# Kernel optimization log

Hardware: AMD Instinct MI355X
Metric: run time of the kernel (lower is better)

## Reference

```python
import jax, jax.numpy as jnp
import numpy as np
import math

B, S, E, H = 2, 2048, 768, 12
D = E // H            # head_dim = 64
FFN = 3072            # GeGLU hidden
WIN = 64              # local window size
GLOBAL_IDS = np.array([0])
EPS = 1e-5


def _rope(x):
    # x: [B,H,S,D]; interleaved rotary embedding, theta=10000 (lucidrains RotaryEmbedding)
    d = x.shape[-1]
    s = x.shape[-2]
    inv_freq = 1.0 / (10000.0 ** (jnp.arange(0, d, 2, dtype=jnp.float32) / d))
    freqs = jnp.arange(s, dtype=jnp.float32)[:, None] * inv_freq[None, :]  # [S, D/2]
    freqs = jnp.repeat(freqs, 2, axis=-1)                                   # [S, D]
    cos, sin = jnp.cos(freqs), jnp.sin(freqs)
    xp = x.reshape(x.shape[:-1] + (d // 2, 2))
    x_rot = jnp.stack([-xp[..., 1], xp[..., 0]], axis=-1).reshape(x.shape)
    return x * cos + x_rot * sin


def _layernorm(x, scale, bias):
    mu = jnp.mean(x, axis=-1, keepdims=True)
    var = jnp.mean(jnp.square(x - mu), axis=-1, keepdims=True)
    return (x - mu) * jax.lax.rsqrt(var + EPS) * scale + bias


def setup_inputs() -> dict:
    key = jax.random.key(0)
    ks = jax.random.split(key, 10)
    def xav(k, shape, gain):
        fan_out, fan_in = shape
        std = gain * math.sqrt(2.0 / (fan_in + fan_out))
        return jax.random.normal(k, shape, jnp.float32) * std
    g2 = math.sqrt(2.0)
    g13 = math.sqrt(1.0 / 3.0)
    return {
        "x": jax.random.normal(ks[0], (B, S, E), jnp.float32),
        "rel_pos_bias": jax.random.normal(ks[1], (B, S, S), jnp.float32),
        "mask": jnp.ones((B, S), dtype=bool),
        "wq_w": xav(ks[2], (E, E), g2), "wq_b": jnp.zeros((E,), jnp.float32),
        "wk_w": xav(ks[3], (E, E), g2), "wk_b": jnp.zeros((E,), jnp.float32),
        "wv_w": xav(ks[4], (E, E), g2), "wv_b": jnp.zeros((E,), jnp.float32),
        "fc_w": xav(ks[5], (E, E), g2), "fc_b": jnp.zeros((E,), jnp.float32),
        "pos_coeff": jnp.full((H, 1, 1), 0.01, jnp.float32),
        "gate_w": xav(ks[6], (FFN, E), g13), "gate_b": jnp.zeros((FFN,), jnp.float32),
        "value_w": xav(ks[7], (FFN, E), g2), "value_b": jnp.zeros((FFN,), jnp.float32),
        "down_w": xav(ks[8], (E, FFN), g2), "down_b": jnp.zeros((E,), jnp.float32),
        "ln1_s": jnp.ones((E,), jnp.float32), "ln1_b": jnp.zeros((E,), jnp.float32),
        "ln2_s": jnp.ones((E,), jnp.float32), "ln2_b": jnp.zeros((E,), jnp.float32),
    }


def _sparse_allow(mask):
    # static local-window + global-token pattern, [S,S] bool
    idx = jnp.arange(S)
    allow = jnp.abs(idx[:, None] - idx[None, :]) <= WIN
    gidx = jnp.asarray(GLOBAL_IDS)
    allow = allow.at[gidx, :].set(True)
    allow = allow.at[:, gidx].set(True)
    # combine with padding mask [B,S] broadcast over query rows
    return allow[None, None, :, :] & mask[:, None, None, :]  # [B,1,S,S]


def reference(x, rel_pos_bias, mask, wq_w, wq_b, wk_w, wk_b, wv_w, wv_b,
              fc_w, fc_b, pos_coeff, gate_w, gate_b, value_w, value_b,
              down_w, down_b, ln1_s, ln1_b, ln2_s, ln2_b):
    def heads(t):  # [B,S,E] -> [B,H,S,D]
        return t.reshape(B, S, H, D).transpose(0, 2, 1, 3)

    Q = _rope(heads(x @ wq_w.T + wq_b))
    K = _rope(heads(x @ wk_w.T + wk_b))
    V = heads(x @ wv_w.T + wv_b)

    scores = jnp.einsum('bhqd,bhkd->bhqk', Q, K) / math.sqrt(D)
    scores = scores + pos_coeff[None] * rel_pos_bias[:, None]     # [B,H,S,S]
    allow = _sparse_allow(mask)
    scores = jnp.where(allow, scores, -1e30)
    scores = scores - jnp.max(scores, axis=-1, keepdims=True)
    attn = jax.nn.softmax(scores, axis=-1)
    ctx = jnp.einsum('bhqk,bhkd->bhqd', attn, V)
    ctx = ctx.transpose(0, 2, 1, 3).reshape(B, S, E)
    attn_out = ctx @ fc_w.T + fc_b

    h = _layernorm(x + attn_out, ln1_s, ln1_b)
    gate = jax.nn.gelu(h @ gate_w.T + gate_b, approximate=False)
    ffn = (gate * (h @ value_w.T + value_b)) @ down_w.T + down_b
    return _layernorm(h + ffn, ln2_s, ln2_b)
```

## Files before the change

### kernel.cpp

```cpp
#include <hip/hip_runtime.h>
#include <math.h>

#define B_   2
#define S_   2048
#define E_   768
#define H_   12
#define D_   64
#define FFN_ 3072
#define WIN_ 64
#define MTOT (B_*S_)

typedef unsigned short ushort_t;
typedef unsigned short ushort8 __attribute__((ext_vector_type(8)));
typedef __bf16 bf16x8 __attribute__((ext_vector_type(8)));
typedef float f32x4 __attribute__((ext_vector_type(4)));
typedef _Float16 half_t;

__device__ __forceinline__ float b2f(ushort_t u) {
    union { unsigned int i; float f; } c; c.i = ((unsigned int)u) << 16; return c.f;
}
__device__ __forceinline__ ushort_t f2b(float f) {
    union { float f; unsigned int i; } c; c.f = f;
    unsigned int u = c.i;
    return (ushort_t)((u + 0x7fffu + ((u >> 16) & 1u)) >> 16);
}
__device__ __forceinline__ float gelu_f(float g) {
    return 0.5f * g * (1.f + erff(g * 0.70710678118654752440f));
}

typedef const __attribute__((address_space(1))) void* gptr_t;
typedef __attribute__((address_space(3))) void* lptr_t;
__device__ __forceinline__ void gload16(const void* g, void* l) {
    __builtin_amdgcn_global_load_lds((gptr_t)g,
        (lptr_t)(unsigned int)(unsigned long long)l, 16, 0, 0);
}

__global__ __launch_bounds__(256)
void cvt_f32_bf16(const float* __restrict__ in, ushort_t* __restrict__ out, int n8)
{
    const int idx = blockIdx.x * 256 + threadIdx.x;
    if (idx >= n8) return;
    const float4* p = (const float4*)(in + (size_t)idx * 8);
    const float4 a = p[0], b = p[1];
    ushort8 o;
    o[0]=f2b(a.x); o[1]=f2b(a.y); o[2]=f2b(a.z); o[3]=f2b(a.w);
    o[4]=f2b(b.x); o[5]=f2b(b.y); o[6]=f2b(b.z); o[7]=f2b(b.w);
    *(ushort8*)(out + (size_t)idx*8) = o;
}

__global__ __launch_bounds__(256)
void cvt_interleave(const float* __restrict__ gw, const float* __restrict__ vw,
                    ushort_t* __restrict__ out)
{
    const int idx = blockIdx.x*256 + threadIdx.x;
    const int R   = idx / 96, c8 = idx - R*96;
    const int blk = R >> 6, w = R & 63;
    const float* src = (w < 32 ? gw : vw) + (size_t)(blk*32 + (w & 31))*768 + c8*8;
    const float4 a = ((const float4*)src)[0], b = ((const float4*)src)[1];
    ushort8 o;
    o[0]=f2b(a.x); o[1]=f2b(a.y); o[2]=f2b(a.z); o[3]=f2b(a.w);
    o[4]=f2b(b.x); o[5]=f2b(b.y); o[6]=f2b(b.z); o[7]=f2b(b.w);
    *(ushort8*)(out + (size_t)idx*8) = o;
}

__global__ __launch_bounds__(256)
void rope_table(float2* __restrict__ ctab)
{
    const int idx = blockIdx.x*256 + threadIdx.x;
    if (idx >= S_*32) return;
    const int s = idx >> 5, i = idx & 31;
    const float inv = exp2f(-(float)i * (13.287712379549449f/32.0f));
    const float fr = (float)s * inv;
    ctab[idx] = make_float2(cosf(fr), sinf(fr));
}

template<int EPI, int BN>
__global__ __launch_bounds__(256)
void gemm_mfma(const ushort_t* __restrict__ A,
               const ushort_t* W0, const float* b0, void* C0,
               const ushort_t* W1, const float* b1, void* C1,
               const ushort_t* W2, const float* b2, void* C2,
               const void* __restrict__ aux, int M, int N, int K)
{
    constexpr int NWC = BN/64, NWR = 4/NWC, WROWS = 128/NWR, MF = WROWS/16;
    const ushort_t* W = W0; const float* bias = b0; void* C = C0;
    if (blockIdx.z == 1) { W = W1; bias = b1; C = C1; }
    else if (blockIdx.z == 2) { W = W2; bias = b2; C = C2; }

    __shared__ __align__(16) ushort_t As[128*32];
    __shared__ __align__(16) ushort_t Bs[BN*32];

    const int tid = threadIdx.x, wv = tid>>6, lane = tid&63;
    const int m0 = blockIdx.y*128, n0 = blockIdx.x*BN;
    const int wr = wv / NWC, wc = wv % NWC;
    const int lr16 = lane & 15, lkb = (lane>>4)<<3;

    f32x4 acc[MF][4];
#pragma unroll
    for (int i=0;i<MF;++i)
#pragma unroll
        for (int j=0;j<4;++j) acc[i][j] = f32x4{0.f,0.f,0.f,0.f};

    const char* Ab = (const char*)(A + (size_t)m0*K);
    const char* Wb = (const char*)(W + (size_t)n0*K);
    const size_t rb = (size_t)K*2;
    const int wbase = wv*1024, lby = lane*16;

    for (int kt = 0; kt < K; kt += 32) {
        const size_t kb = (size_t)kt*2;
        int n_ = wbase + lby;
        gload16(Ab + (size_t)(n_>>6)*rb + kb + (n_&63), (char*)As + wbase);
        n_ += 4096;
        gload16(Ab + (size_t)(n_>>6)*rb + kb + (n_&63), (char*)As + wbase + 4096);
        n_ = wbase + lby;
        gload16(Wb + (size_t)(n_>>6)*rb + kb + (n_&63), (char*)Bs + wbase);
        if (BN == 128) {
            n_ += 4096;
            gload16(Wb + (size_t)(n_>>6)*rb + kb + (n_&63), (char*)Bs + wbase + 4096);
        }
        __syncthreads();
        bf16x8 af[MF], bfr[4];
#pragma unroll
        for (int mf=0; mf<MF; ++mf)
            af[mf] = *(const bf16x8*)&As[(wr*WROWS + mf*16 + lr16)*32 + lkb];
#pragma unroll
        for (int nf=0; nf<4; ++nf)
            bfr[nf] = *(const bf16x8*)&Bs[(wc*64 + nf*16 + lr16)*32 + lkb];
#pragma unroll
        for (int mf=0; mf<MF; ++mf)
#pragma unroll
            for (int nf=0; nf<4; ++nf)
                acc[mf][nf] = __builtin_amdgcn_mfma_f32_16x16x32_bf16(af[mf], bfr[nf], acc[mf][nf], 0,0,0);
        __syncthreads();
    }

    const int colb = n0 + wc*64 + lr16;
    const int rowb = m0 + wr*WROWS + ((lane>>4)<<2);
#pragma unroll
    for (int nf=0; nf<4; ++nf) {
        const int col = colb + nf*16;
        const float bsv = bias[col];
#pragma unroll
        for (int mf=0; mf<MF; ++mf) {
            const int row = rowb + mf*16;
            const f32x4 a = acc[mf][nf];
#pragma unroll
            for (int r=0; r<4; ++r) {
                const size_t off = (size_t)(row+r)*N + col;
                const float v = a[r] + bsv;
                if constexpr (EPI == 0) {
                    ((ushort_t*)C)[off] = f2b(v);
                } else {
                    ((float*)C)[off] = v + ((const float*)aux)[off];
                }
            }
        }
// ... 43 lines not shown

#define STGQ(tt, cb) { \
    char* dA = lds + (cb)*BUFB + wv*2048; \
    char* dB = lds + (cb)*BUFB + ABY + wv*2048; \
    const size_t ko = (size_t)(tt)*64; \
    gload16(Agp + ko,           dA); \
    gload16(Agp + ko + 16*1536, dA + 1024); \
    gload16(Bgp + ko,           dB); \
    gload16(Bgp + ko + 16*1536, dB + 1024); }

    STGQ(0, 0);
    __syncthreads();

    int c = 0;
#pragma unroll 1
    for (int t = 0; t < NT; ++t) {
        if (t < NT-1) STGQ(t+1, c^1);
        const char* Lb = lds + c*BUFB;
        const bf16x8 a0 = *(const bf16x8*)(Lb + rA0 + ck);
        const bf16x8 a1 = *(const bf16x8*)(Lb + rA1 + ck);
        const bf16x8 a2 = *(const bf16x8*)(Lb + rA2 + ck);
        const bf16x8 a3 = *(const bf16x8*)(Lb + rA3 + ck);
        const bf16x8 b0 = *(const bf16x8*)(Lb + rB0 + ck);
        const bf16x8 b1 = *(const bf16x8*)(Lb + rB1 + ck);
        const bf16x8 b2 = *(const bf16x8*)(Lb + rB2 + ck);
        const bf16x8 b3 = *(const bf16x8*)(Lb + rB3 + ck);
        __builtin_amdgcn_s_setprio(1);
        acc[0][0] = __builtin_amdgcn_mfma_f32_16x16x32_bf16(a0, b0, acc[0][0], 0,0,0);
        acc[1][0] = __builtin_amdgcn_mfma_f32_16x16x32_bf16(a1, b0, acc[1][0], 0,0,0);
        acc[2][0] = __builtin_amdgcn_mfma_f32_16x16x32_bf16(a2, b0, acc[2][0], 0,0,0);
        acc[3][0] = __builtin_amdgcn_mfma_f32_16x16x32_bf16(a3, b0, acc[3][0], 0,0,0);
        acc[0][1] = __builtin_amdgcn_mfma_f32_16x16x32_bf16(a0, b1, acc[0][1], 0,0,0);
        acc[1][1] = __builtin_amdgcn_mfma_f32_16x16x32_bf16(a1, b1, acc[1][1], 0,0,0);
        acc[2][1] = __builtin_amdgcn_mfma_f32_16x16x32_bf16(a2, b1, acc[2][1], 0,0,0);
        acc[3][1] = __builtin_amdgcn_mfma_f32_16x16x32_bf16(a3, b1, acc[3][1], 0,0,0);
        acc[0][2] = __builtin_amdgcn_mfma_f32_16x16x32_bf16(a0, b2, acc[0][2], 0,0,0);
        acc[1][2] = __builtin_amdgcn_mfma_f32_16x16x32_bf16(a1, b2, acc[1][2], 0,0,0);
        acc[2][2] = __builtin_amdgcn_mfma_f32_16x16x32_bf16(a2, b2, acc[2][2], 0,0,0);
        acc[3][2] = __builtin_amdgcn_mfma_f32_16x16x32_bf16(a3, b2, acc[3][2], 0,0,0);
        acc[0][3] = __builtin_amdgcn_mfma_f32_16x16x32_bf16(a0, b3, acc[0][3], 0,0,0);
        acc[1][3] = __builtin_amdgcn_mfma_f32_16x16x32_bf16(a1, b3, acc[1][3], 0,0,0);
        acc[2][3] = __builtin_amdgcn_mfma_f32_16x16x32_bf16(a2, b3, acc[2][3], 0,0,0);
        acc[3][3] = __builtin_amdgcn_mfma_f32_16x16x32_bf16(a3, b3, acc[3][3], 0,0,0);
        __builtin_amdgcn_s_setprio(0);
        __syncthreads();
        c ^= 1;
    }
#undef STGQ

    const int tsel = gx / 6;
    const float* bias = (tsel==0) ? bq : (tsel==1) ? bk : bv;
    ushort_t* out = (tsel==0) ? Qb : Kb;
    const int colb = (gx - tsel*6)*128 + wc*64 + lr16;
    const int rowb = m0 + wr*64 + ((l>>4)<<2);
#pragma unroll
    for (int nf=0; nf<4; ++nf) {
        const int col = colb + nf*16;
        const float bsv = bias[col];
#pragma unroll
        for (int mf=0; mf<4; ++mf) {
            const int row = rowb + mf*16;
            const f32x4 a = acc[mf][nf];
#pragma unroll
            for (int r=0; r<4; ++r) {
                const int rr = row + r;
                const float v = a[r] + bsv;
                if (tsel == 2) {
                    const size_t toff =
                        (((size_t)(rr >> 11)*H_ + (col >> 6))*64 + (col & 63))*(size_t)S_ + (rr & (S_-1));
                    Vt[toff] = f2b(v);
                } else {
                    const int s = rr & (S_-1);
                    const float2 cs = ctab[s*32 + ((col & 63) >> 1)];
                    const float p = __shfl_xor(v, 1);
                    const float rot = (col & 1) ? fmaf(v, cs.x,  p*cs.y)
                                                : fmaf(v, cs.x, -p*cs.y);
                    out[(size_t)rr*E_ + col] = f2b(rot);
                }
            }
        }
    }
}

__global__ __launch_bounds__(256, 2)
void gemm_geglu(const ushort_t* __restrict__ A,
                const ushort_t* __restrict__ Wgv,
                const float* __restrict__ bgp,
                const float* __restrict__ bvp,
                ushort_t* __restrict__ C)
{
    constexpr int NT   = 12;
    constexpr int ABY  = 128*128;
    constexpr int BUFB = 2*ABY;
    __shared__ __align__(16) char lds[2*BUFB];

    const int id  = blockIdx.x;
    const int stI = (id & 7)*3 + ((id >> 3) >> 6);
    const int w64 = (id >> 3) & 63;
    const int gy  = (stI/6)*8 + (w64 >> 3);
    const int gx  = (stI%6)*8 + (w64 & 7);
    const int m0 = gy*128, n0 = gx*128;

    const int tid = threadIdx.x, wv = tid>>6, l = tid&63;
    const int wr = wv>>1, wc = wv&1;
    const int lr16 = l & 15, g16b = (l>>4)<<4;
    const int xr = (lr16 & 7) << 4;

    const int lrow = l >> 3;
    const int swzc = ((l & 7) ^ lrow) << 4;
    const char* Agp = (const char*)A   + (size_t)(m0 + wv*32 + lrow)*1536 + swzc;
    const char* Bgp = (const char*)Wgv + (size_t)(n0 + wv*32 + lrow)*1536 + swzc;

    const int rA0 = (wr*64 +  0 + lr16)*128, rA1 = (wr*64 + 16 + lr16)*128;
    const int rA2 = (wr*64 + 32 + lr16)*128, rA3 = (wr*64 + 48 + lr16)*128;
    const int rB0 = ABY + (wc*64 +  0 + lr16)*128, rB1 = ABY + (wc*64 + 16 + lr16)*128;
    const int rB2 = ABY + (wc*64 + 32 + lr16)*128, rB3 = ABY + (wc*64 + 48 + lr16)*128;
    const int ck0 = g16b ^ xr, ck1 = (64 + g16b) ^ xr;

    f32x4 acc[4][4];
#pragma unroll
    for (int i=0;i<4;++i)
#pragma unroll
        for (int j=0;j<4;++j) acc[i][j] = f32x4{0.f,0.f,0.f,0.f};

#define STG(tt, cb) { \
    char* dA = lds + (cb)*BUFB + wv*4096; \
    char* dB = lds + (cb)*BUFB + ABY + wv*4096; \
    const size_t ko = (size_t)(tt)*128; \
    gload16(Agp + ko,           dA); \
    gload16(Agp + ko +  8*1536, dA + 1024); \
    gload16(Agp + ko + 16*1536, dA + 2048); \
    gload16(Agp + ko + 24*1536, dA + 3072); \
    gload16(Bgp + ko,           dB); \
    gload16(Bgp + ko +  8*1536, dB + 1024); \
    gload16(Bgp + ko + 16*1536, dB + 2048); \
    gload16(Bgp + ko + 24*1536, dB + 3072); }

    STG(0, 0);
    __syncthreads();

    int c = 0;
#pragma unroll 1
    for (int t = 0; t < NT; ++t) {
        if (t < NT-1) STG(t+1, c^1);
        const char* Lb = lds + c*BUFB;
        const bf16x8 a0 = *(const bf16x8*)(Lb + rA0 + ck0);
        const bf16x8 a1 = *(const bf16x8*)(Lb + rA1 + ck0);
        const bf16x8 a2 = *(const bf16x8*)(Lb + rA2 + ck0);
        const bf16x8 a3 = *(const bf16x8*)(Lb + rA3 + ck0);
        const bf16x8 b0 = *(const bf16x8*)(Lb + rB0 + ck0);
        const bf16x8 b1 = *(const bf16x8*)(Lb + rB1 + ck0);
        const bf16x8 b2 = *(const bf16x8*)(Lb + rB2 + ck0);
        const bf16x8 b3 = *(const bf16x8*)(Lb + rB3 + ck0);
        const bf16x8 e0 = *(const bf16x8*)(Lb + rA0 + ck1);
        const bf16x8 e1 = *(const bf16x8*)(Lb + rA1 + ck1);
        const bf16x8 e2 = *(const bf16x8*)(Lb + rA2 + ck1);
        const bf16x8 e3 = *(const bf16x8*)(Lb + rA3 + ck1);
        const bf16x8 f0 = *(const bf16x8*)(Lb + rB0 + ck1);
        const bf16x8 f1 = *(const bf16x8*)(Lb + rB1 + ck1);
        const bf16x8 f2 = *(const bf16x8*)(Lb + rB2 + ck1);
        const bf16x8 f3 = *(const bf16x8*)(Lb + rB3 + ck1);
        __builtin_amdgcn_s_setprio(1);
        acc[0][0] = __builtin_amdgcn_mfma_f32_16x16x32_bf16(a0, b0, acc[0][0], 0,0,0);
        acc[1][0] = __builtin_amdgcn_mfma_f32_16x16x32_bf16(a1, b0, acc[1][0], 0,0,0);
        acc[2][0] = __builtin_amdgcn_mfma_f32_16x16x32_bf16(a2, b0, acc[2][0], 0,0,0);
        acc[3][0] = __builtin_amdgcn_mfma_f32_16x16x32_bf16(a3, b0, acc[3][0], 0,0,0);
        acc[0][1] = __builtin_amdgcn_mfma_f32_16x16x32_bf16(a0, b1, acc[0][1], 0,0,0);
        acc[1][1] = __builtin_amdgcn_mfma_f32_16x16x32_bf16(a1, b1, acc[1][1], 0,0,0);
        acc[2][1] = __builtin_amdgcn_mfma_f32_16x16x32_bf16(a2, b1, acc[2][1], 0,0,0);
        acc[3][1] = __builtin_amdgcn_mfma_f32_16x16x32_bf16(a3, b1, acc[3][1], 0,0,0);
        acc[0][2] = __builtin_amdgcn_mfma_f32_16x16x32_bf16(a0, b2, acc[0][2], 0,0,0);
        acc[1][2] = __builtin_amdgcn_mfma_f32_16x16x32_bf16(a1, b2, acc[1][2], 0,0,0);
        acc[2][2] = __builtin_amdgcn_mfma_f32_16x16x32_bf16(a2, b2, acc[2][2], 0,0,0);
        acc[3][2] = __builtin_amdgcn_mfma_f32_16x16x32_bf16(a3, b2, acc[3][2], 0,0,0);
        acc[0][3] = __builtin_amdgcn_mfma_f32_16x16x32_bf16(a0, b3, acc[0][3], 0,0,0);
        acc[1][3] = __builtin_amdgcn_mfma_f32_16x16x32_bf16(a1, b3, acc[1][3], 0,0,0);
        acc[2][3] = __builtin_amdgcn_mfma_f32_16x16x32_bf16(a2, b3, acc[2][3], 0,0,0);
        acc[3][3] = __builtin_amdgcn_mfma_f32_16x16x32_bf16(a3, b3, acc[3][3], 0,0,0);
        acc[0][0] = __builtin_amdgcn_mfma_f32_16x16x32_bf16(e0, f0, acc[0][0], 0,0,0);
// ... 75 lines not shown
    const int rB1 = ABY + (wc*32 + 16 + lr16)*128;
    const int ck0 = g16b ^ xr, ck1 = (64 + g16b) ^ xr;

    f32x4 acc[4][2];
#pragma unroll
    for (int i=0;i<4;++i)
#pragma unroll
        for (int j=0;j<2;++j) acc[i][j] = f32x4{0.f,0.f,0.f,0.f};

#define STGD(tt, cb) { \
    char* dA = lds + (cb)*BUFB + wv*4096; \
    char* dB = lds + (cb)*BUFB + ABY + wv*2048; \
    const size_t ko = (size_t)(tt)*128; \
    gload16(Agp + ko,           dA); \
    gload16(Agp + ko +  8*6144, dA + 1024); \
    gload16(Agp + ko + 16*6144, dA + 2048); \
    gload16(Agp + ko + 24*6144, dA + 3072); \
    gload16(Bgp + ko,           dB); \
    gload16(Bgp + ko +  8*6144, dB + 1024); }

    STGD(0, 0);
    __syncthreads();

    int c = 0;
#pragma unroll 1
    for (int t = 0; t < NT; ++t) {
        if (t < NT-1) STGD(t+1, c^1);
        const char* Lb = lds + c*BUFB;
        const bf16x8 a0 = *(const bf16x8*)(Lb + rA0 + ck0);
        const bf16x8 a1 = *(const bf16x8*)(Lb + rA1 + ck0);
        const bf16x8 a2 = *(const bf16x8*)(Lb + rA2 + ck0);
        const bf16x8 a3 = *(const bf16x8*)(Lb + rA3 + ck0);
        const bf16x8 b0 = *(const bf16x8*)(Lb + rB0 + ck0);
        const bf16x8 b1 = *(const bf16x8*)(Lb + rB1 + ck0);
        const bf16x8 e0 = *(const bf16x8*)(Lb + rA0 + ck1);
        const bf16x8 e1 = *(const bf16x8*)(Lb + rA1 + ck1);
        const bf16x8 e2 = *(const bf16x8*)(Lb + rA2 + ck1);
        const bf16x8 e3 = *(const bf16x8*)(Lb + rA3 + ck1);
        const bf16x8 f0 = *(const bf16x8*)(Lb + rB0 + ck1);
        const bf16x8 f1 = *(const bf16x8*)(Lb + rB1 + ck1);
        __builtin_amdgcn_s_setprio(1);
        acc[0][0] = __builtin_amdgcn_mfma_f32_16x16x32_bf16(a0, b0, acc[0][0], 0,0,0);
        acc[1][0] = __builtin_amdgcn_mfma_f32_16x16x32_bf16(a1, b0, acc[1][0], 0,0,0);
        acc[2][0] = __builtin_amdgcn_mfma_f32_16x16x32_bf16(a2, b0, acc[2][0], 0,0,0);
        acc[3][0] = __builtin_amdgcn_mfma_f32_16x16x32_bf16(a3, b0, acc[3][0], 0,0,0);
        acc[0][1] = __builtin_amdgcn_mfma_f32_16x16x32_bf16(a0, b1, acc[0][1], 0,0,0);
        acc[1][1] = __builtin_amdgcn_mfma_f32_16x16x32_bf16(a1, b1, acc[1][1], 0,0,0);
        acc[2][1] = __builtin_amdgcn_mfma_f32_16x16x32_bf16(a2, b1, acc[2][1], 0,0,0);
        acc[3][1] = __builtin_amdgcn_mfma_f32_16x16x32_bf16(a3, b1, acc[3][1], 0,0,0);
        acc[0][0] = __builtin_amdgcn_mfma_f32_16x16x32_bf16(e0, f0, acc[0][0], 0,0,0);
        acc[1][0] = __builtin_amdgcn_mfma_f32_16x16x32_bf16(e1, f0, acc[1][0], 0,0,0);
        acc[2][0] = __builtin_amdgcn_mfma_f32_16x16x32_bf16(e2, f0, acc[2][0], 0,0,0);
        acc[3][0] = __builtin_amdgcn_mfma_f32_16x16x32_bf16(e3, f0, acc[3][0], 0,0,0);
        acc[0][1] = __builtin_amdgcn_mfma_f32_16x16x32_bf16(e0, f1, acc[0][1], 0,0,0);
        acc[1][1] = __builtin_amdgcn_mfma_f32_16x16x32_bf16(e1, f1, acc[1][1], 0,0,0);
        acc[2][1] = __builtin_amdgcn_mfma_f32_16x16x32_bf16(e2, f1, acc[2][1], 0,0,0);
        acc[3][1] = __builtin_amdgcn_mfma_f32_16x16x32_bf16(e3, f1, acc[3][1], 0,0,0);
        __builtin_amdgcn_s_setprio(0);
        __syncthreads();
        c ^= 1;
    }
#undef STGD

    const int colb = n0 + wc*32 + lr16;
    const int rowb = m0 + wr*64 + ((l>>4)<<2);
#pragma unroll
    for (int nf=0; nf<2; ++nf) {
        const int col = colb + nf*16;
        const float bsv = bias[col];
#pragma unroll
        for (int mf=0; mf<4; ++mf) {
            const int row = rowb + mf*16;
            const f32x4 a = acc[mf][nf];
#pragma unroll
            for (int rr=0; rr<4; ++rr) {
                const size_t off = (size_t)(row+rr)*E_ + col;
                if (z == 0) P0[off] = a[rr] + bsv;
                else        P1[off] = (half_t)a[rr];
            }
        }
    }
}

__global__ __launch_bounds__(256)
void attn_mfma(const ushort_t* __restrict__ Qb, const ushort_t* __restrict__ Kb,
               const ushort_t* __restrict__ Vt, const float* __restrict__ rel,
               const float* __restrict__ pos_coeff, ushort_t* __restrict__ ctx)
{
    __shared__ __align__(16) ushort_t P_lds[4][16][160];
    const int id = blockIdx.x;
    const int h  = id % H_;
    const int qb = (id / H_) & 31;
    const int b  = id / (H_*32);
    const int wv = threadIdx.x >> 6, l = threadIdx.x & 63;
    const int qw = qb*64 + wv*16;
    const int g  = l >> 4, ql = l & 15;
    const int q  = qw + ql;

    int klo = qw - 64;
    if (klo < 0) klo = 0;
    if (klo > S_-160) klo = S_-160;
    const bool addg = (klo > 0);
    const float pc = pos_coeff[h];

    const ushort_t* qbp = Qb + ((size_t)(b*S_ + qw))*E_ + h*D_ + (size_t)ql*E_ + g*8;
    const bf16x8 qf0 = *(const bf16x8*)(qbp);
    const bf16x8 qf1 = *(const bf16x8*)(qbp + 32);

    float sg = -1e30f, pg = 0.f;
    const float* relrow = rel + ((size_t)(b*S_ + q))*S_;
    if (addg) {
        const ushort_t* k0p = Kb + (size_t)(b*S_)*E_ + h*D_ + g*8;
        const bf16x8 k00 = *(const bf16x8*)(k0p);
        const bf16x8 k01 = *(const bf16x8*)(k0p + 32);
        float part = 0.f;
#pragma unroll
        for (int t = 0; t < 8; ++t) {
            part = fmaf((float)k00[t], (float)qf0[t], part);
            part = fmaf((float)k01[t], (float)qf1[t], part);
        }
        part += __shfl_xor(part, 16);
        part += __shfl_xor(part, 32);
        sg = part*0.125f + pc*relrow[0];
    }

    f32x4 sc_[10];
#pragma unroll
    for (int f = 0; f < 10; ++f) sc_[f] = f32x4{0.f,0.f,0.f,0.f};
    const ushort_t* kbp = Kb + ((size_t)(b*S_ + klo))*E_ + h*D_;
#pragma unroll
    for (int f = 0; f < 10; ++f) {
        const ushort_t* kr = kbp + (size_t)(16*f + ql)*E_ + g*8;
        const bf16x8 kf0 = *(const bf16x8*)(kr);
        const bf16x8 kf1 = *(const bf16x8*)(kr + 32);
        sc_[f] = __builtin_amdgcn_mfma_f32_16x16x32_bf16(kf0, qf0, sc_[f], 0,0,0);
        sc_[f] = __builtin_amdgcn_mfma_f32_16x16x32_bf16(kf1, qf1, sc_[f], 0,0,0);
    }

#pragma unroll
    for (int f = 0; f < 10; ++f) {
#pragma unroll
        for (int r = 0; r < 4; ++r) {
            const int slot = 16*f + 4*g + r;
            const int key  = klo + slot;
            const int dd   = key - q;
            const bool ok  = (dd <= WIN_ && dd >= -WIN_) || (key == 0);
            const float v  = sc_[f][r]*0.125f + pc*relrow[key];
            sc_[f][r] = ok ? v : -1e30f;
        }
    }

    float mx = sg;
#pragma unroll
    for (int f = 0; f < 10; ++f)
#pragma unroll
        for (int r = 0; r < 4; ++r) mx = fmaxf(mx, sc_[f][r]);
    mx = fmaxf(mx, __shfl_xor(mx, 16));
    mx = fmaxf(mx, __shfl_xor(mx, 32));

    float ls = 0.f;
#pragma unroll
    for (int f = 0; f < 10; ++f)
#pragma unroll
        for (int r = 0; r < 4; ++r) {
            const float p = __expf(sc_[f][r] - mx);
            sc_[f][r] = p; ls += p;
        }
    if (addg) pg = __expf(sg - mx);
    ls += (g == 0) ? pg : 0.f;
    ls += __shfl_xor(ls, 16);
    ls += __shfl_xor(ls, 32);
    const float inv = 1.f / ls;

#pragma unroll
    for (int f = 0; f < 10; ++f)
#pragma unroll
        for (int r = 0; r < 4; ++r)
            P_lds[wv][ql][16*f + 4*g + r] = f2b(sc_[f][r]);
    __syncthreads();

    f32x4 acc_c[4];
#pragma unroll
    for (int df = 0; df < 4; ++df) acc_c[df] = f32x4{0.f,0.f,0.f,0.f};
    const ushort_t* vtb = Vt + ((size_t)(b*H_ + h)*64)*(size_t)S_;
#pragma unroll
    for (int s5 = 0; s5 < 5; ++s5) {
        const bf16x8 pf = *(const bf16x8*)&P_lds[wv][ql][32*s5 + 8*g];
#pragma unroll
        for (int df = 0; df < 4; ++df) {
            const bf16x8 vtf = *(const bf16x8*)(vtb + (size_t)(df*16 + ql)*S_ + klo + 32*s5 + g*8);
            acc_c[df] = __builtin_amdgcn_mfma_f32_16x16x32_bf16(vtf, pf, acc_c[df], 0,0,0);
        }
    }

    if (addg) {
#pragma unroll
        for (int df = 0; df < 4; ++df)
#pragma unroll
            for (int r = 0; r < 4; ++r)
                acc_c[df][r] = fmaf(pg, b2f(vtb[(size_t)(df*16 + g*4 + r)*S_]), acc_c[df][r]);
    }

    if (q != 0) {
        ushort_t* cb = ctx + ((size_t)(b*S_ + q))*E_ + h*D_;
#pragma unroll
        for (int df = 0; df < 4; ++df)
#pragma unroll
            for (int r = 0; r < 4; ++r)
                cb[df*16 + g*4 + r] = f2b(acc_c[df][r] * inv);
    }
}

__global__ __launch_bounds__(256)
void attn_global(const ushort_t* __restrict__ Qb, const ushort_t* __restrict__ Kb,
                 const ushort_t* __restrict__ Vt, const float* __restrict__ rel,
                 const float* __restrict__ pos_coeff, ushort_t* __restrict__ ctx)
{
    __shared__ float sc[S_];
    __shared__ float sq[D_];
    __shared__ float red[4];
    __shared__ float pacc[4][D_];
    const int tid = threadIdx.x, wv = tid>>6, lane = tid&63;
    const int id = blockIdx.x, h = id % H_, b = id / H_;

    if (tid < 64) sq[tid] = b2f(Qb[(size_t)(b*S_)*E_ + h*D_ + tid]);
    __syncthreads();

    const float pc = pos_coeff[h];
    const ushort_t* kbase = Kb + (size_t)b*S_*E_ + h*D_;
    const float* relrow = rel + (size_t)b*S_*S_;
    const int g = lane >> 2, sl = lane & 3;

    for (int jb = wv*16; jb < S_; jb += 64) {
        const int j = jb + g;
        const ushort_t* kr = kbase + (size_t)j*E_ + sl*16;
        const ushort8 k0 = *(const ushort8*)kr;
        const ushort8 k1 = *(const ushort8*)(kr + 8);
        const float* qv = &sq[sl*16];
        float partial = 0.f;
#pragma unroll
        for (int t = 0; t < 8; ++t) partial = fmaf(b2f(k0[t]), qv[t], partial);
#pragma unroll
        for (int t = 0; t < 8; ++t) partial = fmaf(b2f(k1[t]), qv[t+8], partial);
        partial += __shfl_xor(partial, 1);
        partial += __shfl_xor(partial, 2);
        if (sl == 0) sc[j] = partial*0.125f + pc*relrow[j];
    }
    __syncthreads();

    float mx = -1e30f;
#pragma unroll
    for (int i = 0; i < 8; ++i) mx = fmaxf(mx, sc[tid + 256*i]);
#pragma unroll
    for (int off = 32; off > 0; off >>= 1) mx = fmaxf(mx, __shfl_xor(mx, off));
    if (lane == 0) red[wv] = mx;
    __syncthreads();
    mx = fmaxf(fmaxf(red[0], red[1]), fmaxf(red[2], red[3]));

    float sum = 0.f;
#pragma unroll
    for (int i = 0; i < 8; ++i) {
        const float p = __expf(sc[tid + 256*i] - mx);
        sc[tid + 256*i] = p; sum += p;
    }
#pragma unroll
    for (int off = 32; off > 0; off >>= 1) sum += __shfl_xor(sum, off);
    __syncthreads();
    if (lane == 0) red[wv] = sum;
    __syncthreads();
    const float inv = 1.f / (red[0]+red[1]+red[2]+red[3]);

    const ushort_t* vtrow = Vt + ((size_t)(b*H_ + h)*64 + lane)*(size_t)S_;
    float acc = 0.f;
    for (int j0 = wv*512; j0 < wv*512 + 512; j0 += 8) {
        const ushort8 v8 = *(const ushort8*)&vtrow[j0];
#pragma unroll
        for (int t = 0; t < 8; ++t) acc = fmaf(sc[j0+t], b2f(v8[t]), acc);
    }
    pacc[wv][lane] = acc;
    __syncthreads();
    if (tid < 64) {
        const float r = (pacc[0][tid]+pacc[1][tid]+pacc[2][tid]+pacc[3][tid]) * inv;
        ctx[(size_t)(b*S_)*E_ + h*D_ + tid] = f2b(r);
    }
}

template<bool WB>
__global__ __launch_bounds__(256)
void ln_kernel(const float* __restrict__ in, const float* __restrict__ gam,
               const float* __restrict__ bet, float* __restrict__ out,
               ushort_t* __restrict__ outb)
{
    const int row = blockIdx.x;
    const float* r = in + (size_t)row * E_;
    const int tid = threadIdx.x;
    const float v0 = r[tid], v1 = r[tid+256], v2 = r[tid+512];
    float s  = v0+v1+v2;
    float ss = v0*v0+v1*v1+v2*v2;
#pragma unroll
    for (int off = 32; off > 0; off >>= 1) {
        s  += __shfl_xor(s, off);
        ss += __shfl_xor(ss, off);
    }
    __shared__ float rs[4], rss[4];
    const int wv = tid >> 6, lane = tid & 63;
    if (lane == 0) { rs[wv] = s; rss[wv] = ss; }
    __syncthreads();
    s  = rs[0]+rs[1]+rs[2]+rs[3];
    ss = rss[0]+rss[1]+rss[2]+rss[3];
    const float mu  = s * (1.f/E_);
    const float var = ss * (1.f/E_) - mu*mu;
    const float rstd = rsqrtf(var + 1e-5f);
    float* o = out + (size_t)row * E_;
    const float o0 = (v0-mu)*rstd*gam[tid    ] + bet[tid    ];
    const float o1 = (v1-mu)*rstd*gam[tid+256] + bet[tid+256];
    const float o2 = (v2-mu)*rstd*gam[tid+512] + bet[tid+512];
    o[tid] = o0; o[tid+256] = o1; o[tid+512] = o2;
    if constexpr (WB) {
        ushort_t* ob = outb + (size_t)row * E_;
        ob[tid] = f2b(o0); ob[tid+256] = f2b(o1); ob[tid+512] = f2b(o2);
    }
}

__global__ __launch_bounds__(256)
void ln3_kernel(const float* __restrict__ p0, const half_t* __restrict__ p1,
                const float* __restrict__ res, const float* __restrict__ gam,
                const float* __restrict__ bet, float* __restrict__ out)
{
    const int row = blockIdx.x;
    const size_t base = (size_t)row * E_;
    const int tid = threadIdx.x;
    const float v0 = p0[base+tid]     + (float)p1[base+tid]     + res[base+tid];
    const float v1 = p0[base+tid+256] + (float)p1[base+tid+256] + res[base+tid+256];
    const float v2 = p0[base+tid+512] + (float)p1[base+tid+512] + res[base+tid+512];
    float s  = v0+v1+v2;
    float ss = v0*v0+v1*v1+v2*v2;
#pragma unroll
    for (int off = 32; off > 0; off >>= 1) {
        s  += __shfl_xor(s, off);
        ss += __shfl_xor(ss, off);
    }
    __shared__ float rs[4], rss[4];
    const int wv = tid >> 6, lane = tid & 63;
    if (lane == 0) { rs[wv] = s; rss[wv] = ss; }
    __syncthreads();
    s  = rs[0]+rs[1]+rs[2]+rs[3];
    ss = rss[0]+rss[1]+rss[2]+rss[3];
    const float mu  = s * (1.f/E_);
    const float var = ss * (1.f/E_) - mu*mu;
    const float rstd = rsqrtf(var + 1e-5f);
    float* o = out + base;
    o[tid]     = (v0-mu)*rstd*gam[tid    ] + bet[tid    ];
    o[tid+256] = (v1-mu)*rstd*gam[tid+256] + bet[tid+256];
    o[tid+512] = (v2-mu)*rstd*gam[tid+512] + bet[tid+512];
}

extern "C" void kernel_launch(void* const* d_in, const int* in_sizes, int n_in,
                              void* d_out, int out_size, void* d_ws, size_t ws_size,
                              hipStream_t stream)
{
    const float* x      = (const float*)d_in[0];
    const float* rel    = (const float*)d_in[1];
    const float* wq_w   = (const float*)d_in[3];
    const float* wq_b   = (const float*)d_in[4];
    const float* wk_w   = (const float*)d_in[5];
    const float* wk_b   = (const float*)d_in[6];
    const float* wv_w   = (const float*)d_in[7];
    const float* wv_b   = (const float*)d_in[8];
    const float* fc_w   = (const float*)d_in[9];
    const float* fc_b   = (const float*)d_in[10];
    const float* pos_c  = (const float*)d_in[11];
    const float* gate_w = (const float*)d_in[12];
    const float* gate_b = (const float*)d_in[13];
    const float* value_w= (const float*)d_in[14];
    const float* value_b= (const float*)d_in[15];
    const float* down_w = (const float*)d_in[16];
    const float* down_b = (const float*)d_in[17];
    const float* ln1_s  = (const float*)d_in[18];
    const float* ln1_b  = (const float*)d_in[19];
    const float* ln2_s  = (const float*)d_in[20];
    const float* ln2_b  = (const float*)d_in[21];
    float* out = (float*)d_out;

    char* W = (char*)d_ws;
    ushort_t* Qb     = (ushort_t*)(W + 0);
    ushort_t* Kb     = (ushort_t*)(W + 6291456);
    ushort_t* Vt     = (ushort_t*)(W + 12582912);
    ushort_t* Cxb    = (ushort_t*)(W + 18874368);
    ushort_t* GpB    = (ushort_t*)(W + 0);
    ushort_t* Xb     = (ushort_t*)(W + 25165824);
    ushort_t* wqb    = (ushort_t*)(W + 31457280);
    ushort_t* wkb    = (ushort_t*)(W + 32636928);
    ushort_t* wvb    = (ushort_t*)(W + 33816576);
    ushort_t* fcb    = (ushort_t*)(W + 34996224);
    ushort_t* Wgv    = (ushort_t*)(W + 25165824);
    ushort_t* downb  = (ushort_t*)(W + 34996224);
    float*    AO     = (float*)   (W + 39714816);
    float*    Hb     = (float*)   (W + 52297728);
    ushort_t* Hbb    = (ushort_t*)(W + 64880640);
    half_t*   P1h    = (half_t*)  (W + 64880640);
    float2*   ctab   = (float2*)  (W + 71172096);

    cvt_f32_bf16<<<1536, 256, 0, stream>>>(x, Xb, MTOT*E_/8);
    cvt_f32_bf16<<<288,  256, 0, stream>>>(wq_w, wqb, E_*E_/8);
    cvt_f32_bf16<<<288,  256, 0, stream>>>(wk_w, wkb, E_*E_/8);
    cvt_f32_bf16<<<288,  256, 0, stream>>>(wv_w, wvb, E_*E_/8);
    cvt_f32_bf16<<<288,  256, 0, stream>>>(fc_w, fcb, E_*E_/8);
    rope_table<<<(S_*32+255)/256, 256, 0, stream>>>(ctab);

    gemm_qkv<<<576, 256, 0, stream>>>(Xb, wqb, wq_b, wk_b, wv_b, ctab, Qb, Kb, Vt);

    cvt_interleave<<<2304, 256, 0, stream>>>(gate_w, value_w, Wgv);

    attn_mfma<<<B_*H_*(S_/64), 256, 0, stream>>>(Qb, Kb, Vt, rel, pos_c, Cxb);
    attn_global<<<B_*H_, 256, 0, stream>>>(Qb, Kb, Vt, rel, pos_c, Cxb);

    gemm_mfma<1,64><<<dim3(E_/64, MTOT/128, 1), 256, 0, stream>>>(
        Cxb, fcb, fc_b, AO, nullptr, nullptr, nullptr, nullptr, nullptr, nullptr,
        x, MTOT, E_, E_);

    cvt_f32_bf16<<<1152, 256, 0, stream>>>(down_w, downb, E_*FFN_/8);

    ln_kernel<true><<<MTOT, 256, 0, stream>>>(AO, ln1_s, ln1_b, Hb, Hbb);

    gemm_geglu<<<dim3(1536), 256, 0, stream>>>(Hbb, Wgv, gate_b, value_b, GpB);

    gemm_down<<<dim3(768), 256, 0, stream>>>(GpB, downb, down_b, AO, P1h);

    ln3_kernel<<<MTOT, 256, 0, stream>>>(AO, P1h, Hb, ln2_s, ln2_b, out);
}
```

Baseline: 236.3 us.

## Merge conversion and attention launches into fewer multi-role kernels

Folds the six prep launches (input/weight bf16 conversions and RoPE table) into one block-indexed kernel. The local attention, global-token attention and gate/value weight interleave become one launch, and the down-weight conversion rides on extra blocks of the GeGLU GEMM. The aim is to cut launch overhead and let small independent jobs fill idle compute units. In exchange, blocks of different roles share one launch configuration, so the GEMM kernel's LDS footprint and occupancy limit now also apply to the cheap conversion blocks.

```diff
diff --git a/kernel.cpp b/kernel.cpp
--- a/kernel.cpp
+++ b/kernel.cpp
@@ -35,11 +35,9 @@
         (lptr_t)(unsigned int)(unsigned long long)l, 16, 0, 0);
 }
 
-__global__ __launch_bounds__(256)
-void cvt_f32_bf16(const float* __restrict__ in, ushort_t* __restrict__ out, int n8)
-{
-    const int idx = blockIdx.x * 256 + threadIdx.x;
-    if (idx >= n8) return;
+__device__ __forceinline__ void cvt8(const float* __restrict__ in,
+                                     ushort_t* __restrict__ out, int idx)
+{
     const float4* p = (const float4*)(in + (size_t)idx * 8);
     const float4 a = p[0], b = p[1];
     ushort8 o;
@@ -49,29 +47,31 @@
 }
 
 __global__ __launch_bounds__(256)
-void cvt_interleave(const float* __restrict__ gw, const float* __restrict__ vw,
-                    ushort_t* __restrict__ out)
-{
-    const int idx = blockIdx.x*256 + threadIdx.x;
-    const int R   = idx / 96, c8 = idx - R*96;
-    const int blk = R >> 6, w = R & 63;
-    const float* src = (w < 32 ? gw : vw) + (size_t)(blk*32 + (w & 31))*768 + c8*8;
-    const float4 a = ((const float4*)src)[0], b = ((const float4*)src)[1];
-    ushort8 o;
-    o[0]=f2b(a.x); o[1]=f2b(a.y); o[2]=f2b(a.z); o[3]=f2b(a.w);
-    o[4]=f2b(b.x); o[5]=f2b(b.y); o[6]=f2b(b.z); o[7]=f2b(b.w);
-    *(ushort8*)(out + (size_t)idx*8) = o;
-}
-
-__global__ __launch_bounds__(256)
-void rope_table(float2* __restrict__ ctab)
-{
-    const int idx = blockIdx.x*256 + threadIdx.x;
-    if (idx >= S_*32) return;
-    const int s = idx >> 5, i = idx & 31;
-    const float inv = exp2f(-(float)i * (13.287712379549449f/32.0f));
-    const float fr = (float)s * inv;
-    ctab[idx] = make_float2(cosf(fr), sinf(fr));
+void prep_fused(const float* __restrict__ x,
+                const float* __restrict__ wq_w, const float* __restrict__ wk_w,
+                const float* __restrict__ wv_w, const float* __restrict__ fc_w,
+                ushort_t* __restrict__ Xb, ushort_t* __restrict__ wqb,
+                ushort_t* __restrict__ wkb, ushort_t* __restrict__ wvb,
+                ushort_t* __restrict__ fcb, float2* __restrict__ ctab)
+{
+    const int id = blockIdx.x, tid = threadIdx.x;
+    if (id < 1536) {
+        cvt8(x, Xb, id*256 + tid);
+    } else if (id < 1824) {
+        cvt8(wq_w, wqb, (id-1536)*256 + tid);
+    } else if (id < 2112) {
+        cvt8(wk_w, wkb, (id-1824)*256 + tid);
+    } else if (id < 2400) {
+        cvt8(wv_w, wvb, (id-2112)*256 + tid);
+    } else if (id < 2688) {
+        cvt8(fc_w, fcb, (id-2400)*256 + tid);
+    } else {
+        const int idx = (id-2688)*256 + tid;
+        const int s = idx >> 5, i = idx & 31;
+        const float inv = exp2f(-(float)i * (13.287712379549449f/32.0f));
+        const float fr = (float)s * inv;
+        ctab[idx] = make_float2(cosf(fr), sinf(fr));
+    }
 }
 
 template<int EPI, int BN>
@@ -281,12 +281,232 @@
     }
 }
 
+__global__ __launch_bounds__(256)
+void attn_fused(const ushort_t* __restrict__ Qb, const ushort_t* __restrict__ Kb,
+                const ushort_t* __restrict__ Vt, const float* __restrict__ rel,
+                const float* __restrict__ pos_coeff, ushort_t* __restrict__ ctx,
+                const float* __restrict__ gw, const float* __restrict__ vw,
+                ushort_t* __restrict__ Wgv)
+{
+    __shared__ __align__(16) char smem[20480];
+    const int bid = blockIdx.x;
+
+    if (bid >= 792) {
+        const int idx = (bid - 792)*256 + threadIdx.x;
+        const int R   = idx / 96, c8 = idx - R*96;
+        const int blk = R >> 6, w = R & 63;
+        const float* src = (w < 32 ? gw : vw) + (size_t)(blk*32 + (w & 31))*768 + c8*8;
+        const float4 a = ((const float4*)src)[0], b = ((const float4*)src)[1];
+        ushort8 o;
+        o[0]=f2b(a.x); o[1]=f2b(a.y); o[2]=f2b(a.z); o[3]=f2b(a.w);
+        o[4]=f2b(b.x); o[5]=f2b(b.y); o[6]=f2b(b.z); o[7]=f2b(b.w);
+        *(ushort8*)(Wgv + (size_t)idx*8) = o;
+        return;
+    }
+
+    if (bid >= 768) {
+        float* sc = (float*)smem;
+        float* sq = (float*)(smem + 8192);
+        float* red = (float*)(smem + 8448);
+        float (*pacc)[D_] = (float(*)[D_])(smem + 8464);
+        const int tid = threadIdx.x, wv = tid>>6, lane = tid&63;
+        const int gid = bid - 768, h = gid % H_, b = gid / H_;
+
+        if (tid < 64) sq[tid] = b2f(Qb[(size_t)(b*S_)*E_ + h*D_ + tid]);
+        __syncthreads();
+
+        const float pc = pos_coeff[h];
+        const ushort_t* kbase = Kb + (size_t)b*S_*E_ + h*D_;
+        const float* relrow = rel + (size_t)b*S_*S_;
+        const int g = lane >> 2, sl = lane & 3;
+
+        for (int jb = wv*16; jb < S_; jb += 64) {
+            const int j = jb + g;
+            const ushort_t* kr = kbase + (size_t)j*E_ + sl*16;
+            const ushort8 k0 = *(const ushort8*)kr;
+            const ushort8 k1 = *(const ushort8*)(kr + 8);
+            const float* qv = &sq[sl*16];
+            float partial = 0.f;
+#pragma unroll
+            for (int t = 0; t < 8; ++t) partial = fmaf(b2f(k0[t]), qv[t], partial);
+#pragma unroll
+            for (int t = 0; t < 8; ++t) partial = fmaf(b2f(k1[t]), qv[t+8], partial);
+            partial += __shfl_xor(partial, 1);
+            partial += __shfl_xor(partial, 2);
+            if (sl == 0) sc[j] = partial*0.125f + pc*relrow[j];
+        }
+        __syncthreads();
+
+        float mx = -1e30f;
+#pragma unroll
+        for (int i = 0; i < 8; ++i) mx = fmaxf(mx, sc[tid + 256*i]);
+#pragma unroll
+        for (int off = 32; off > 0; off >>= 1) mx = fmaxf(mx, __shfl_xor(mx, off));
+        if (lane == 0) red[wv] = mx;
+        __syncthreads();
+        mx = fmaxf(fmaxf(red[0], red[1]), fmaxf(red[2], red[3]));
+
+        float sum = 0.f;
+#pragma unroll
+        for (int i = 0; i < 8; ++i) {
+            const float p = __expf(sc[tid + 256*i] - mx);
+            sc[tid + 256*i] = p; sum += p;
+        }
+#pragma unroll
+        for (int off = 32; off > 0; off >>= 1) sum += __shfl_xor(sum, off);
+        __syncthreads();
+        if (lane == 0) red[wv] = sum;
+        __syncthreads();
+        const float inv = 1.f / (red[0]+red[1]+red[2]+red[3]);
+
+        const ushort_t* vtrow = Vt + ((size_t)(b*H_ + h)*64 + lane)*(size_t)S_;
+        float acc = 0.f;
+        for (int j0 = wv*512; j0 < wv*512 + 512; j0 += 8) {
+            const ushort8 v8 = *(const ushort8*)&vtrow[j0];
+#pragma unroll
+            for (int t = 0; t < 8; ++t) acc = fmaf(sc[j0+t], b2f(v8[t]), acc);
+        }
+        pacc[wv][lane] = acc;
+        __syncthreads();
+        if (tid < 64) {
+            const float r = (pacc[0][tid]+pacc[1][tid]+pacc[2][tid]+pacc[3][tid]) * inv;
+            ctx[(size_t)(b*S_)*E_ + h*D_ + tid] = f2b(r);
+        }
+        return;
+    }
+
+    ushort_t (*P_lds)[16][160] = reinterpret_cast<ushort_t(*)[16][160]>(smem);
+    const int id = bid;
+    const int h  = id % H_;
+    const int qb = (id / H_) & 31;
+    const int b  = id / (H_*32);
+    const int wv = threadIdx.x >> 6, l = threadIdx.x & 63;
+    const int qw = qb*64 + wv*16;
+    const int g  = l >> 4, ql = l & 15;
+    const int q  = qw + ql;
+
+    int klo = qw - 64;
+    if (klo < 0) klo = 0;
+    if (klo > S_-160) klo = S_-160;
+    const bool addg = (klo > 0);
+    const float pc = pos_coeff[h];
+
+    const ushort_t* qbp = Qb + ((size_t)(b*S_ + qw))*E_ + h*D_ + (size_t)ql*E_ + g*8;
+    const bf16x8 qf0 = *(const bf16x8*)(qbp);
+    const bf16x8 qf1 = *(const bf16x8*)(qbp + 32);
+
+    float sg = -1e30f, pg = 0.f;
+    const float* relrow = rel + ((size_t)(b*S_ + q))*S_;
+    if (addg) {
+        const ushort_t* k0p = Kb + (size_t)(b*S_)*E_ + h*D_ + g*8;
+        const bf16x8 k00 = *(const bf16x8*)(k0p);
+        const bf16x8 k01 = *(const bf16x8*)(k0p + 32);
+        float part = 0.f;
+#pragma unroll
+        for (int t = 0; t < 8; ++t) {
+            part = fmaf((float)k00[t], (float)qf0[t], part);
+            part = fmaf((float)k01[t], (float)qf1[t], part);
+        }
+        part += __shfl_xor(part, 16);
+        part += __shfl_xor(part, 32);
+        sg = part*0.125f + pc*relrow[0];
+    }
+
+    f32x4 sc_[10];
+#pragma unroll
+    for (int f = 0; f < 10; ++f) sc_[f] = f32x4{0.f,0.f,0.f,0.f};
+    const ushort_t* kbp = Kb + ((size_t)(b*S_ + klo))*E_ + h*D_;
+#pragma unroll
+    for (int f = 0; f < 10; ++f) {
+        const ushort_t* kr = kbp + (size_t)(16*f + ql)*E_ + g*8;
+        const bf16x8 kf0 = *(const bf16x8*)(kr);
+        const bf16x8 kf1 = *(const bf16x8*)(kr + 32);
+        sc_[f] = __builtin_amdgcn_mfma_f32_16x16x32_bf16(kf0, qf0, sc_[f], 0,0,0);
+        sc_[f] = __builtin_amdgcn_mfma_f32_16x16x32_bf16(kf1, qf1, sc_[f], 0,0,0);
+    }
+
+#pragma unroll
+    for (int f = 0; f < 10; ++f) {
+#pragma unroll
+        for (int r = 0; r < 4; ++r) {
+            const int slot = 16*f + 4*g + r;
+            const int key  = klo + slot;
+            const int dd   = key - q;
+            const bool ok  = (dd <= WIN_ && dd >= -WIN_) || (key == 0);
+            const float v  = sc_[f][r]*0.125f + pc*relrow[key];
+            sc_[f][r] = ok ? v : -1e30f;
+        }
+    }
+
+    float mx = sg;
+#pragma unroll
+    for (int f = 0; f < 10; ++f)
+#pragma unroll
+        for (int r = 0; r < 4; ++r) mx = fmaxf(mx, sc_[f][r]);
+    mx = fmaxf(mx, __shfl_xor(mx, 16));
+    mx = fmaxf(mx, __shfl_xor(mx, 32));
+
+    float ls = 0.f;
+#pragma unroll
+    for (int f = 0; f < 10; ++f)
+#pragma unroll
+        for (int r = 0; r < 4; ++r) {
+            const float p = __expf(sc_[f][r] - mx);
+            sc_[f][r] = p; ls += p;
+        }
+    if (addg) pg = __expf(sg - mx);
+    ls += (g == 0) ? pg : 0.f;
+    ls += __shfl_xor(ls, 16);
+    ls += __shfl_xor(ls, 32);
+    const float inv = 1.f / ls;
+
+#pragma unroll
+    for (int f = 0; f < 10; ++f)
+#pragma unroll
+        for (int r = 0; r < 4; ++r)
+            P_lds[wv][ql][16*f + 4*g + r] = f2b(sc_[f][r]);
+    __syncthreads();
+
+    f32x4 acc_c[4];
+#pragma unroll
+    for (int df = 0; df < 4; ++df) acc_c[df] = f32x4{0.f,0.f,0.f,0.f};
+    const ushort_t* vtb = Vt + ((size_t)(b*H_ + h)*64)*(size_t)S_;
+#pragma unroll
+    for (int s5 = 0; s5 < 5; ++s5) {
+        const bf16x8 pf = *(const bf16x8*)&P_lds[wv][ql][32*s5 + 8*g];
+#pragma unroll
+        for (int df = 0; df < 4; ++df) {
+            const bf16x8 vtf = *(const bf16x8*)(vtb + (size_t)(df*16 + ql)*S_ + klo + 32*s5 + g*8);
+            acc_c[df] = __builtin_amdgcn_mfma_f32_16x16x32_bf16(vtf, pf, acc_c[df], 0,0,0);
+        }
+    }
+
+    if (addg) {
+#pragma unroll
+        for (int df = 0; df < 4; ++df)
+#pragma unroll
+            for (int r = 0; r < 4; ++r)
+                acc_c[df][r] = fmaf(pg, b2f(vtb[(size_t)(df*16 + g*4 + r)*S_]), acc_c[df][r]);
+    }
+
+    if (q != 0) {
+        ushort_t* cb = ctx + ((size_t)(b*S_ + q))*E_ + h*D_;
+#pragma unroll
+        for (int df = 0; df < 4; ++df)
+#pragma unroll
+            for (int r = 0; r < 4; ++r)
+                cb[df*16 + g*4 + r] = f2b(acc_c[df][r] * inv);
+    }
+}
+
 __global__ __launch_bounds__(256, 2)
 void gemm_geglu(const ushort_t* __restrict__ A,
                 const ushort_t* __restrict__ Wgv,
                 const float* __restrict__ bgp,
                 const float* __restrict__ bvp,
-                ushort_t* __restrict__ C)
+                ushort_t* __restrict__ C,
+                const float* __restrict__ down_w,
+                ushort_t* __restrict__ downb)
 {
     constexpr int NT   = 12;
     constexpr int ABY  = 128*128;
@@ -294,6 +514,10 @@
     __shared__ __align__(16) char lds[2*BUFB];
 
     const int id  = blockIdx.x;
+    if (id >= 1536) {
+        cvt8(down_w, downb, (id-1536)*256 + threadIdx.x);
+        return;
+    }
     const int stI = (id & 7)*3 + ((id >> 3) >> 6);
     const int w64 = (id >> 3) & 63;
     const int gy  = (stI/6)*8 + (w64 >> 3);
@@ -535,209 +759,6 @@
     }
 }
 
-__global__ __launch_bounds__(256)
-void attn_mfma(const ushort_t* __restrict__ Qb, const ushort_t* __restrict__ Kb,
-               const ushort_t* __restrict__ Vt, const float* __restrict__ rel,
-               const float* __restrict__ pos_coeff, ushort_t* __restrict__ ctx)
-{
-    __shared__ __align__(16) ushort_t P_lds[4][16][160];
-    const int id = blockIdx.x;
-    const int h  = id % H_;
-    const int qb = (id / H_) & 31;
-    const int b  = id / (H_*32);
-    const int wv = threadIdx.x >> 6, l = threadIdx.x & 63;
-    const int qw = qb*64 + wv*16;
-    const int g  = l >> 4, ql = l & 15;
-    const int q  = qw + ql;
-
-    int klo = qw - 64;
-    if (klo < 0) klo = 0;
-    if (klo > S_-160) klo = S_-160;
-    const bool addg = (klo > 0);
-    const float pc = pos_coeff[h];
-
-    const ushort_t* qbp = Qb + ((size_t)(b*S_ + qw))*E_ + h*D_ + (size_t)ql*E_ + g*8;
-    const bf16x8 qf0 = *(const bf16x8*)(qbp);
-    const bf16x8 qf1 = *(const bf16x8*)(qbp + 32);
-
-    float sg = -1e30f, pg = 0.f;
-    const float* relrow = rel + ((size_t)(b*S_ + q))*S_;
-    if (addg) {
-        const ushort_t* k0p = Kb + (size_t)(b*S_)*E_ + h*D_ + g*8;
-        const bf16x8 k00 = *(const bf16x8*)(k0p);
-        const bf16x8 k01 = *(const bf16x8*)(k0p + 32);
-        float part = 0.f;
-#pragma unroll
-        for (int t = 0; t < 8; ++t) {
-            part = fmaf((float)k00[t], (float)qf0[t], part);
-            part = fmaf((float)k01[t], (float)qf1[t], part);
-        }
-        part += __shfl_xor(part, 16);
-        part += __shfl_xor(part, 32);
-        sg = part*0.125f + pc*relrow[0];
-    }
-
-    f32x4 sc_[10];
-#pragma unroll
-    for (int f = 0; f < 10; ++f) sc_[f] = f32x4{0.f,0.f,0.f,0.f};
-    const ushort_t* kbp = Kb + ((size_t)(b*S_ + klo))*E_ + h*D_;
-#pragma unroll
-    for (int f = 0; f < 10; ++f) {
-        const ushort_t* kr = kbp + (size_t)(16*f + ql)*E_ + g*8;
-        const bf16x8 kf0 = *(const bf16x8*)(kr);
-        const bf16x8 kf1 = *(const bf16x8*)(kr + 32);
-        sc_[f] = __builtin_amdgcn_mfma_f32_16x16x32_bf16(kf0, qf0, sc_[f], 0,0,0);
-        sc_[f] = __builtin_amdgcn_mfma_f32_16x16x32_bf16(kf1, qf1, sc_[f], 0,0,0);
-    }
-
-#pragma unroll
-    for (int f = 0; f < 10; ++f) {
-#pragma unroll
-        for (int r = 0; r < 4; ++r) {
-            const int slot = 16*f + 4*g + r;
-            const int key  = klo + slot;
-            const int dd   = key - q;
-            const bool ok  = (dd <= WIN_ && dd >= -WIN_) || (key == 0);
-            const float v  = sc_[f][r]*0.125f + pc*relrow[key];
-            sc_[f][r] = ok ? v : -1e30f;
-        }
-    }
-
-    float mx = sg;
-#pragma unroll
-    for (int f = 0; f < 10; ++f)
-#pragma unroll
-        for (int r = 0; r < 4; ++r) mx = fmaxf(mx, sc_[f][r]);
-    mx = fmaxf(mx, __shfl_xor(mx, 16));
-    mx = fmaxf(mx, __shfl_xor(mx, 32));
-
-    float ls = 0.f;
-#pragma unroll
-    for (int f = 0; f < 10; ++f)
-#pragma unroll
-        for (int r = 0; r < 4; ++r) {
-            const float p = __expf(sc_[f][r] - mx);
-            sc_[f][r] = p; ls += p;
-        }
-    if (addg) pg = __expf(sg - mx);
-    ls += (g == 0) ? pg : 0.f;
-    ls += __shfl_xor(ls, 16);
-    ls += __shfl_xor(ls, 32);
-    const float inv = 1.f / ls;
-
-#pragma unroll
-    for (int f = 0; f < 10; ++f)
-#pragma unroll
-        for (int r = 0; r < 4; ++r)
-            P_lds[wv][ql][16*f + 4*g + r] = f2b(sc_[f][r]);
-    __syncthreads();
-
-    f32x4 acc_c[4];
-#pragma unroll
-    for (int df = 0; df < 4; ++df) acc_c[df] = f32x4{0.f,0.f,0.f,0.f};
-    const ushort_t* vtb = Vt + ((size_t)(b*H_ + h)*64)*(size_t)S_;
-#pragma unroll
-    for (int s5 = 0; s5 < 5; ++s5) {
-        const bf16x8 pf = *(const bf16x8*)&P_lds[wv][ql][32*s5 + 8*g];
-#pragma unroll
-        for (int df = 0; df < 4; ++df) {
-            const bf16x8 vtf = *(const bf16x8*)(vtb + (size_t)(df*16 + ql)*S_ + klo + 32*s5 + g*8);
-            acc_c[df] = __builtin_amdgcn_mfma_f32_16x16x32_bf16(vtf, pf, acc_c[df], 0,0,0);
-        }
-    }
-
-    if (addg) {
-#pragma unroll
-        for (int df = 0; df < 4; ++df)
-#pragma unroll
-            for (int r = 0; r < 4; ++r)
-                acc_c[df][r] = fmaf(pg, b2f(vtb[(size_t)(df*16 + g*4 + r)*S_]), acc_c[df][r]);
-    }
-
-    if (q != 0) {
-        ushort_t* cb = ctx + ((size_t)(b*S_ + q))*E_ + h*D_;
-#pragma unroll
-        for (int df = 0; df < 4; ++df)
-#pragma unroll
-            for (int r = 0; r < 4; ++r)
-                cb[df*16 + g*4 + r] = f2b(acc_c[df][r] * inv);
-    }
-}
-
-__global__ __launch_bounds__(256)
-void attn_global(const ushort_t* __restrict__ Qb, const ushort_t* __restrict__ Kb,
-                 const ushort_t* __restrict__ Vt, const float* __restrict__ rel,
-                 const float* __restrict__ pos_coeff, ushort_t* __restrict__ ctx)
-{
-    __shared__ float sc[S_];
-    __shared__ float sq[D_];
-    __shared__ float red[4];
-    __shared__ float pacc[4][D_];
-    const int tid = threadIdx.x, wv = tid>>6, lane = tid&63;
-    const int id = blockIdx.x, h = id % H_, b = id / H_;
-
-    if (tid < 64) sq[tid] = b2f(Qb[(size_t)(b*S_)*E_ + h*D_ + tid]);
-    __syncthreads();
-
-    const float pc = pos_coeff[h];
-    const ushort_t* kbase = Kb + (size_t)b*S_*E_ + h*D_;
-    const float* relrow = rel + (size_t)b*S_*S_;
-    const int g = lane >> 2, sl = lane & 3;
-
-    for (int jb = wv*16; jb < S_; jb += 64) {
-        const int j = jb + g;
-        const ushort_t* kr = kbase + (size_t)j*E_ + sl*16;
-        const ushort8 k0 = *(const ushort8*)kr;
-        const ushort8 k1 = *(const ushort8*)(kr + 8);
-        const float* qv = &sq[sl*16];
-        float partial = 0.f;
-#pragma unroll
-        for (int t = 0; t < 8; ++t) partial = fmaf(b2f(k0[t]), qv[t], partial);
-#pragma unroll
-        for (int t = 0; t < 8; ++t) partial = fmaf(b2f(k1[t]), qv[t+8], partial);
-        partial += __shfl_xor(partial, 1);
-        partial += __shfl_xor(partial, 2);
-        if (sl == 0) sc[j] = partial*0.125f + pc*relrow[j];
-    }
-    __syncthreads();
-
-    float mx = -1e30f;
-#pragma unroll
-    for (int i = 0; i < 8; ++i) mx = fmaxf(mx, sc[tid + 256*i]);
-#pragma unroll
-    for (int off = 32; off > 0; off >>= 1) mx = fmaxf(mx, __shfl_xor(mx, off));
-    if (lane == 0) red[wv] = mx;
-    __syncthreads();
-    mx = fmaxf(fmaxf(red[0], red[1]), fmaxf(red[2], red[3]));
-
-    float sum = 0.f;
-#pragma unroll
-    for (int i = 0; i < 8; ++i) {
-        const float p = __expf(sc[tid + 256*i] - mx);
-        sc[tid + 256*i] = p; sum += p;
-    }
-#pragma unroll
-    for (int off = 32; off > 0; off >>= 1) sum += __shfl_xor(sum, off);
-    __syncthreads();
-    if (lane == 0) red[wv] = sum;
-    __syncthreads();
-    const float inv = 1.f / (red[0]+red[1]+red[2]+red[3]);
-
-    const ushort_t* vtrow = Vt + ((size_t)(b*H_ + h)*64 + lane)*(size_t)S_;
-    float acc = 0.f;
-    for (int j0 = wv*512; j0 < wv*512 + 512; j0 += 8) {
-        const ushort8 v8 = *(const ushort8*)&vtrow[j0];
-#pragma unroll
-        for (int t = 0; t < 8; ++t) acc = fmaf(sc[j0+t], b2f(v8[t]), acc);
-    }
-    pacc[wv][lane] = acc;
-    __syncthreads();
-    if (tid < 64) {
-        const float r = (pacc[0][tid]+pacc[1][tid]+pacc[2][tid]+pacc[3][tid]) * inv;
-        ctx[(size_t)(b*S_)*E_ + h*D_ + tid] = f2b(r);
-    }
-}
-
 template<bool WB>
 __global__ __launch_bounds__(256)
 void ln_kernel(const float* __restrict__ in, const float* __restrict__ gam,
@@ -854,29 +875,22 @@
     half_t*   P1h    = (half_t*)  (W + 64880640);
     float2*   ctab   = (float2*)  (W + 71172096);
 
-    cvt_f32_bf16<<<1536, 256, 0, stream>>>(x, Xb, MTOT*E_/8);
-    cvt_f32_bf16<<<288,  256, 0, stream>>>(wq_w, wqb, E_*E_/8);
-    cvt_f32_bf16<<<288,  256, 0, stream>>>(wk_w, wkb, E_*E_/8);
-    cvt_f32_bf16<<<288,  256, 0, stream>>>(wv_w, wvb, E_*E_/8);
-    cvt_f32_bf16<<<288,  256, 0, stream>>>(fc_w, fcb, E_*E_/8);
-    rope_table<<<(S_*32+255)/256, 256, 0, stream>>>(ctab);
+    prep_fused<<<2944, 256, 0, stream>>>(x, wq_w, wk_w, wv_w, fc_w,
+                                         Xb, wqb, wkb, wvb, fcb, ctab);
 
     gemm_qkv<<<576, 256, 0, stream>>>(Xb, wqb, wq_b, wk_b, wv_b, ctab, Qb, Kb, Vt);
 
-    cvt_interleave<<<2304, 256, 0, stream>>>(gate_w, value_w, Wgv);
-
-    attn_mfma<<<B_*H_*(S_/64), 256, 0, stream>>>(Qb, Kb, Vt, rel, pos_c, Cxb);
-    attn_global<<<B_*H_, 256, 0, stream>>>(Qb, Kb, Vt, rel, pos_c, Cxb);
+    attn_fused<<<3096, 256, 0, stream>>>(Qb, Kb, Vt, rel, pos_c, Cxb,
+                                         gate_w, value_w, Wgv);
 
     gemm_mfma<1,64><<<dim3(E_/64, MTOT/128, 1), 256, 0, stream>>>(
         Cxb, fcb, fc_b, AO, nullptr, nullptr, nullptr, nullptr, nullptr, nullptr,
         x, MTOT, E_, E_);
 
-    cvt_f32_bf16<<<1152, 256, 0, stream>>>(down_w, downb, E_*FFN_/8);
-
     ln_kernel<true><<<MTOT, 256, 0, stream>>>(AO, ln1_s, ln1_b, Hb, Hbb);
 
-    gemm_geglu<<<dim3(1536), 256, 0, stream>>>(Hbb, Wgv, gate_b, value_b, GpB);
+    gemm_geglu<<<dim3(2688), 256, 0, stream>>>(Hbb, Wgv, gate_b, value_b, GpB,
+                                               down_w, downb);
 
     gemm_down<<<dim3(768), 256, 0, stream>>>(GpB, downb, down_b, AO, P1h);
 
```

Measured after the change: 217.2 us. 1.09x faster.
